# Optimization experiments

Measured on AMD Instinct MI355X. Metric: run time of the kernel, lower is better.

## Reference

```python
import jax, jax.numpy as jnp
import numpy as np

N = 729        # problem variables
B = 8          # batch
K = 32         # mixing rank (hard-coded in MixingFunc)
NB = 40        # number of symmetry-basis matrices
MAX_ITER = 10  # coordinate-descent sweeps


def setup_inputs() -> dict:
    key = jax.random.key(0)
    ks = jax.random.split(key, 7)
    coeff = jax.random.normal(ks[0], (NB,), jnp.float32)
    upper = jax.random.normal(ks[1], (N,), jnp.float32)
    basis = jax.random.normal(ks[2], (NB, N, N), jnp.float32)
    z = jax.random.uniform(ks[3], (B, N), jnp.float32)
    is_input = jax.random.randint(ks[4], (B, N), 0, 2).astype(jnp.int32)
    v_init_raw = jax.random.normal(ks[5], (B, N + 1, K), jnp.float32)
    # random permutation of the N non-truth variables (indices 1..N), as in satnet init
    perm = (jax.random.permutation(ks[6], N) + 1).astype(jnp.int32)
    return dict(coeff=coeff, upper=upper, basis=basis, z=z,
                is_input=is_input, v_init_raw=v_init_raw, perm=perm)


def _build_C(coeff, upper, basis):
    # BasisFunc.forward: C = [[0, upper^T], [upper, sum_b coeff_b * basis_b]]
    center = jnp.einsum('b,bij->ij', coeff, basis)              # (N, N)
    top = jnp.concatenate([jnp.zeros((1,), upper.dtype), upper])[None, :]  # (1, N+1)
    bottom = jnp.concatenate([upper[:, None], center], axis=1)  # (N, N+1)
    return jnp.concatenate([top, bottom], axis=0)               # (N+1, N+1)


def _init_V(v_raw, z_full):
    # SATNet init: v0 = random unit truth direction; each v_i is placed on the
    # cone around v0 at angle pi*z_i using a random orthogonal direction.
    v0 = v_raw[:, 0] / jnp.linalg.norm(v_raw[:, 0], axis=-1, keepdims=True)  # (B, K)
    dot = jnp.einsum('bnk,bk->bn', v_raw, v0)
    u = v_raw - dot[..., None] * v0[:, None, :]
    u = u / jnp.maximum(jnp.linalg.norm(u, axis=-1, keepdims=True), 1e-8)
    c = jnp.cos(jnp.pi * z_full)[..., None]
    s = jnp.sin(jnp.pi * z_full)[..., None]
    V = -c * v0[:, None, :] + s * u                              # (B, N+1, K)
    V = V.at[:, 0].set(v0)                                       # truth vector pinned
    return V


def _mix(C, V, is_input_full, perm):
    # SATNet mixing coordinate descent: for each free variable i,
    #   g_i = sum_j C[j,i] v_j - C[i,i] v_i ;  v_i <- -g_i / ||g_i||
    Cdiag = jnp.diagonal(C)
    free = (is_input_full == 0)                                  # (B, N+1)

    def coord_step(V, i):
        g = jnp.einsum('j,bjk->bk', C[:, i], V) - Cdiag[i] * V[:, i]  # (B, K)
        gn = jnp.linalg.norm(g, axis=-1, keepdims=True)
        vnew = -g / jnp.maximum(gn, 1e-8)
        V = V.at[:, i].set(jnp.where(free[:, i][:, None], vnew, V[:, i]))
        return V, None

    def sweep(V, _):
        V, _ = jax.lax.scan(coord_step, V, perm)
        return V, None

    V, _ = jax.lax.scan(jax.checkpoint(sweep), V, None, length=MAX_ITER)
    return V


def reference(coeff, upper, basis, z, is_input, v_init_raw, perm):
    Bn = z.shape[0]
    C = _build_C(coeff, upper, basis)
    z_full = jnp.concatenate([jnp.ones((Bn, 1), z.dtype), z], axis=1)
    ii_full = jnp.concatenate(
        [jnp.ones((Bn, 1), is_input.dtype), is_input], axis=1)
    V = _init_V(v_init_raw, z_full)
    V = _mix(C, V, ii_full, perm)
    v0 = V[:, 0]
    cosang = jnp.clip(-jnp.einsum('bnk,bk->bn', V, v0), -1.0 + 1e-6, 1.0 - 1e-6)
    zo = jnp.arccos(cosang) / jnp.pi
    z_out = jnp.where(ii_full == 1, z_full, zo)
    return z_out[:, 1:]
```

## Files before the change

kernel.cpp:

```cpp
#include <hip/hip_runtime.h>

#define NN   729
#define NF   730
#define BV   8
#define KK   32
#define NBAS 40
#define MAXIT 10
#define PI_F 3.14159265358979323846f

#define MTH   512
#define BT    16
#define AST   448
#define NMT   28

typedef short v8s __attribute__((ext_vector_type(8)));
typedef float v4f __attribute__((ext_vector_type(4)));

__device__ __forceinline__ unsigned short f2bf(float f) {
    unsigned int x = __float_as_uint(f);
    unsigned int r = x + 0x7FFFu + ((x >> 16) & 1u);
    return (unsigned short)(r >> 16);
}

__global__ void build_C_kernel(const float* __restrict__ coeff,
                               const float* __restrict__ upper,
                               const float* __restrict__ basis,
                               float* __restrict__ Ct) {
    int idx = blockIdx.x * blockDim.x + threadIdx.x;
    if (idx >= NF * NF) return;
    int i = idx / NF, j = idx - i * NF;
    float val;
    if (i == 0) {
        val = (j == 0) ? 0.f : upper[j - 1];
    } else if (j == 0) {
        val = upper[i - 1];
    } else {
        float acc = 0.f;
        const float* bp = basis + (size_t)(i - 1) * NN + (j - 1);
        #pragma unroll 8
        for (int b = 0; b < NBAS; ++b)
            acc = fmaf(coeff[b], bp[(size_t)b * NN * NN], acc);
        val = acc;
    }
    Ct[(size_t)j * NF + i] = val;
}

__global__ void init_V_kernel(const float* __restrict__ z,
                              const float* __restrict__ vraw,
                              float* __restrict__ V) {
    int g = threadIdx.x >> 5;
    int k = threadIdx.x & 31;
    int row = blockIdx.x * 8 + g;
    int b = row / NF, n = row - b * NF;
    const float* vr = vraw + (size_t)b * NF * KK;

    float v0 = vr[k];
    float s2 = v0 * v0;
    #pragma unroll
    for (int off = 16; off; off >>= 1) s2 += __shfl_xor(s2, off, 32);
    v0 = v0 / sqrtf(s2);

    float vn = vr[(size_t)n * KK + k];
    float d = vn * v0;
    #pragma unroll
    for (int off = 16; off; off >>= 1) d += __shfl_xor(d, off, 32);
    float u = vn - d * v0;
    float un2 = u * u;
    #pragma unroll
    for (int off = 16; off; off >>= 1) un2 += __shfl_xor(un2, off, 32);
    u = u / fmaxf(sqrtf(un2), 1e-8f);

    float zf = (n == 0) ? 1.f : z[b * NN + (n - 1)];
    float c = cosf(PI_F * zf), s = sinf(PI_F * zf);
    float outv = -c * v0 + s * u;
    if (n == 0) outv = v0;
    V[((size_t)b * NF + n) * KK + k] = outv;
}

__global__ void build_act_kernel(const int* __restrict__ is_input,
                                 const int* __restrict__ perm,
                                 int* __restrict__ act, int* __restrict__ nA_arr) {
    int b = blockIdx.x, l = threadIdx.x;
    int base = 0;
    for (int c = 0; c < (NN + 63) / 64; ++c) {
        int idx = c * 64 + l;
        bool f = false; int pi = 0;
        if (idx < NN) { pi = perm[idx]; f = (is_input[b * NN + pi - 1] == 0); }
        unsigned long long m = __ballot(f);
        int pos = __popcll(m & ((1ull << l) - 1ull));
        if (f && base + pos < AST) act[b * AST + base + pos] = pi;
        base += __popcll(m);
    }
    if (base > AST) base = AST;
    if (l == 0) nA_arr[b] = base;
    for (int p = base + l; p < AST; p += 64) act[b * AST + p] = 0;
}

__global__ void init_W_kernel(const float* __restrict__ Ct,
                              const int* __restrict__ act,
                              const int* __restrict__ nA_arr,
                              const float* __restrict__ V,
                              float* __restrict__ Wc,
                              float* __restrict__ Vact) {
    int b = blockIdx.y;
    int a = blockIdx.x * 8 + (threadIdx.x >> 5);
    int k = threadIdx.x & 31;
    int nA = nA_arr[b];
    float w = 0.f;
    int ra = act[b * AST + a];
    float vv = V[((size_t)b * NF + ra) * KK + k];
    if (a < nA) {
        const float* ctr = Ct + (size_t)ra * NF;
        const float* vb = V + (size_t)b * NF * KK + k;
        float acc = 0.f;
        for (int j = 0; j < NF; ++j)
            acc = fmaf(ctr[j], vb[(size_t)j * KK], acc);
        w = acc - ctr[ra] * vv;
    }
    Wc[((size_t)b * AST + a) * KK + k] = w;
    Vact[((size_t)b * AST + a) * KK + k] = vv;
}

__global__ void prepack_A_kernel(const float* __restrict__ Ct,
                                 const int* __restrict__ act,
                                 v8s* __restrict__ Apack) {
    int b = blockIdx.y, pm = blockIdx.x;
    int pb = pm / NMT, mt = pm - NMT * pb;
    int l = threadIdx.x;
    if (l >= 32) return;
    int row = mt * 16 + (l & 15);
    int ra = act[b * AST + row];
    const float* crow = Ct + (size_t)ra * NF;
    v8s v;
    #pragma unroll
    for (int i = 0; i < 8; ++i) {
        int t = (l >> 4) * 8 + i;
        int rt = act[b * AST + pb * 16 + t];
        v[i] = (short)f2bf(crow[rt]);
    }
    Apack[(((size_t)b * NMT + pb) * NMT + mt) * 32 + l] = v;
}

__device__ __forceinline__ float rowsum16(float x) {
    int y;
    y = __builtin_amdgcn_update_dpp(0, __float_as_int(x), 0x121, 0xF, 0xF, false);
    x += __int_as_float(y);
    y = __builtin_amdgcn_update_dpp(0, __float_as_int(x), 0x122, 0xF, 0xF, false);
    x += __int_as_float(y);
    y = __builtin_amdgcn_update_dpp(0, __float_as_int(x), 0x124, 0xF, 0xF, false);
    x += __int_as_float(y);
    y = __builtin_amdgcn_update_dpp(0, __float_as_int(x), 0x128, 0xF, 0xF, false);
    x += __int_as_float(y);
    return x;
}

__global__ __launch_bounds__(MTH, 2)
void mix_kernel(const v8s* __restrict__ Apack_g,
                const float* __restrict__ Ct_g,
                const float* __restrict__ Wc_g,
                const float* __restrict__ Vact_g,
                const int* __restrict__ act_g,
                const int* __restrict__ nA_arr,
                const int* __restrict__ is_input,
                const float* __restrict__ z,
                const float* __restrict__ Vg,
                float* __restrict__ out) {
    __shared__ __align__(16) float V_c[AST * KK];
    __shared__ __align__(16) float dv_s[2][BT * KK];
    __shared__ __align__(16) float gpub[2][BT * KK];
    __shared__ __align__(16) float cblk_s[2][BT * BT];
    __shared__ __align__(16) float cmini_s[BT * BT];
    __shared__ float Cd_s[AST];
    __shared__ int   slot_s[NF];
    __shared__ int   act_s[AST];

    int b = blockIdx.x, tid = threadIdx.x;
    const v8s* Apack = Apack_g + ((size_t)b * NMT * NMT) * 32;
    const float* Vact = Vact_g + (size_t)b * AST * KK;
    int nA = nA_arr[b];
    int nblkp = (nA + BT - 1) / BT;
    if (nblkp < 2) nblkp = 2;
    if (nblkp > NMT) nblkp = NMT;
    int totB = MAXIT * nblkp;

    int wid = tid >> 6;
    int l64 = tid & 63;
    int col = l64 & 15, rg = l64 >> 4;
    int k32 = tid & 31;

    if (tid < AST) act_s[tid] = act_g[b * AST + tid];
    __syncthreads();
    for (int idx = tid; idx < AST * 8; idx += MTH)
        ((float4*)V_c)[idx] = ((const float4*)Vact)[idx];
    if (tid < AST) Cd_s[tid] = Ct_g[(size_t)act_s[tid] * NF + act_s[tid]];
    if (tid < nA) slot_s[act_s[tid]] = tid;
    if (tid < 256) {
        int t = tid >> 4, u = tid & 15;
        cblk_s[0][t * BT + u] = Ct_g[(size_t)act_s[u] * NF + act_s[t]];
    }
    v4f acc[4][2];
    #pragma unroll
    for (int tl = 0; tl < 4; ++tl)
        #pragma unroll
        for (int nt = 0; nt < 2; ++nt) {
            v4f z4 = {0.f, 0.f, 0.f, 0.f};
            acc[tl][nt] = z4;
        }
    if (wid >= 1) {
        #pragma unroll
        for (int tl = 0; tl < 4; ++tl) {
            int mt = (wid - 1) * 4 + tl;
            #pragma unroll
            for (int nt = 0; nt < 2; ++nt)
                #pragma unroll
                for (int i = 0; i < 4; ++i)
                    acc[tl][nt][i] =
                        Wc_g[((size_t)b * AST + mt * 16 + rg * 4 + i) * KK + nt * 16 + col];
        }
        if (wid == 1) {
            #pragma unroll
            for (int nt = 0; nt < 2; ++nt)
                #pragma unroll
                for (int i = 0; i < 4; ++i)
                    gpub[1][(rg * 4 + i) * KK + nt * 16 + col] = acc[0][nt][i];
        }
    }
    __syncthreads();

    for (int bi = 0; bi < totB; ++bi) {
        int blk = bi % nblkp, s0 = blk * BT;
        int pblk = (bi - 1 + nblkp) % nblkp, sp0 = pblk * BT;
        int cb = bi & 1, pv = cb ^ 1;
        int nblk2 = (bi + 1) % nblkp, sn0 = nblk2 * BT;

        if (wid == 0) {
            __builtin_amdgcn_s_setprio(1);
            float g[BT], vo[BT];
            #pragma unroll
            for (int u = 0; u < BT; ++u) {
                g[u]  = gpub[pv][u * KK + k32];
                vo[u] = V_c[(s0 + u) * KK + k32];
            }
            #pragma unroll
            for (int u = 0; u < BT; ++u) {
                int s = s0 + u;
                float n2 = g[u] * g[u];
                n2 = rowsum16(n2);
                n2 += __shfl_xor(n2, 16, 32);
                float inv = -__builtin_amdgcn_rsqf(fmaxf(n2, 1e-16f));
                float msk = (s < nA) ? 1.f : 0.f;
                float d = fmaf(g[u], inv, -vo[u]) * msk;
                if (tid < 32) {
                    dv_s[cb][u * KK + k32] = d;
                    V_c[s * KK + k32] = vo[u] + d;
                }
                #pragma unroll
                for (int u2 = u + 1; u2 < BT; ++u2)
                    g[u2] = fmaf(cblk_s[cb][u * BT + u2], d, g[u2]);
            }
            __builtin_amdgcn_s_setprio(0);
        } else {
            if (wid == 6) {
                for (int idx = l64; idx < BT * BT; idx += 64) {
                    int u = idx >> 4, t = idx & 15;
                    cmini_s[u * BT + t] =
                        Ct_g[(size_t)act_s[sn0 + u] * NF + act_s[s0 + t]];
                }
            }
            if (wid == 7) {
                for (int idx = l64; idx < BT * BT; idx += 64) {
                    int x = idx >> 4, y = idx & 15;
                    cblk_s[pv][idx] =
                        Ct_g[(size_t)act_s[sn0 + y] * NF + act_s[sn0 + x]];
                }
            }
            if (bi > 0) {
                v8s bf0, bf1;
                #pragma unroll
                for (int i = 0; i < 8; ++i) { bf0[i] = 0; bf1[i] = 0; }
                if (l64 < 32) {
                    #pragma unroll
                    for (int i = 0; i < 8; ++i) {
                        int t = rg * 8 + i;
                        bf0[i] = (short)f2bf(dv_s[pv][t * KK + col]);
                        bf1[i] = (short)f2bf(dv_s[pv][t * KK + 16 + col]);
                    }
                }
                #pragma unroll
                for (int tl = 0; tl < 4; ++tl) {
                    int mt = (wid - 1) * 4 + tl;
                    v8s af;
                    #pragma unroll
                    for (int i = 0; i < 8; ++i) af[i] = 0;
                    if (l64 < 32)
                        af = Apack[((size_t)pblk * NMT + mt) * 32 + l64];
                    acc[tl][0] = __builtin_amdgcn_mfma_f32_16x16x32_bf16(af, bf0, acc[tl][0], 0, 0, 0);
                    acc[tl][1] = __builtin_amdgcn_mfma_f32_16x16x32_bf16(af, bf1, acc[tl][1], 0, 0, 0);
                }
                #pragma unroll
                for (int tl = 0; tl < 4; ++tl) {
                    if ((wid - 1) * 4 + tl == pblk) {
                        #pragma unroll
                        for (int i = 0; i < 4; ++i) {
                            int r = rg * 4 + i;
                            float cd = Cd_s[sp0 + r];
                            acc[tl][0][i] = fmaf(-cd, dv_s[pv][r * KK + col],      acc[tl][0][i]);
                            acc[tl][1][i] = fmaf(-cd, dv_s[pv][r * KK + 16 + col], acc[tl][1][i]);
                        }
                    }
                }
            }
            #pragma unroll
            for (int tl = 0; tl < 4; ++tl) {
                if ((wid - 1) * 4 + tl == nblk2) {
                    #pragma unroll
                    for (int i = 0; i < 4; ++i) {
                        gpub[cb][(rg * 4 + i) * KK + col]      = acc[tl][0][i];
                        gpub[cb][(rg * 4 + i) * KK + 16 + col] = acc[tl][1][i];
                    }
                }
            }
        }
        __syncthreads();

        {
            int u = tid >> 5, k = tid & 31;
            float g = gpub[cb][u * KK + k];
            #pragma unroll
            for (int t = 0; t < BT; ++t)
                g = fmaf(cmini_s[u * BT + t], dv_s[cb][t * KK + k], g);
            gpub[cb][u * KK + k] = g;
        }
        __syncthreads();
    }

    int k = tid & 31, r = tid >> 5;
    float v0k = Vg[(size_t)b * NF * KK + k];
    for (int n = 1 + r; n <= NN; n += 16) {
        int ii = is_input[b * NN + n - 1];
        float res;
        if (ii == 1) {
            res = z[b * NN + n - 1];
        } else {
            int a = slot_s[n];
            float dot = V_c[a * KK + k] * v0k;
            #pragma unroll
            for (int off = 16; off; off >>= 1) dot += __shfl_xor(dot, off, 32);
            float ca = fminf(fmaxf(-dot, -1.f + 1e-6f), 1.f - 1e-6f);
            res = acosf(ca) * (1.f / PI_F);
        }
        if (k == 0) out[b * NN + n - 1] = res;
    }
}

extern "C" void kernel_launch(void* const* d_in, const int* in_sizes, int n_in,
                              void* d_out, int out_size, void* d_ws, size_t ws_size,
                              hipStream_t stream) {
    const float* coeff    = (const float*)d_in[0];
    const float* upper    = (const float*)d_in[1];
    const float* basis    = (const float*)d_in[2];
    const float* z        = (const float*)d_in[3];
    const int*   is_input = (const int*)d_in[4];
    const float* vraw     = (const float*)d_in[5];
    const int*   perm     = (const int*)d_in[6];
    float* out = (float*)d_out;

    float* ws   = (float*)d_ws;
    float* Ct   = ws;
    float* V    = Ct + (size_t)NF * NF;
    float* Wc   = V + (size_t)BV * NF * KK;
    float* Vact = Wc + (size_t)BV * AST * KK;
    int*   act  = (int*)(Vact + (size_t)BV * AST * KK);
    int*   nAa  = act + BV * AST;
    v8s*  Apack = (v8s*)(nAa + 8);

    build_C_kernel<<<dim3((NF * NF + 255) / 256), dim3(256), 0, stream>>>(coeff, upper, basis, Ct);
    init_V_kernel<<<dim3(730), dim3(256), 0, stream>>>(z, vraw, V);
    build_act_kernel<<<dim3(BV), dim3(64), 0, stream>>>(is_input, perm, act, nAa);
    init_W_kernel<<<dim3(AST / 8, BV), dim3(256), 0, stream>>>(Ct, act, nAa, V, Wc, Vact);
    prepack_A_kernel<<<dim3(NMT * NMT, BV), dim3(64), 0, stream>>>(Ct, act, Apack);
    mix_kernel<<<dim3(BV), dim3(MTH), 0, stream>>>(Apack, Ct, Wc, Vact, act, nAa, is_input, z, V, out);
}
```

Measured before the change: 722.5 us.

## Double the coordinate-block size to 32 so MFMA uses full K width

Raises the sequential coordinate block from 16 to 32 variables, halving the number of block iterations and the __syncthreads barriers per sweep. The A-panel prepack now fills all 64 lanes, so the 16x16x32 bf16 MFMA uses its full K=32 instead of zero-padding half of it. The serial wave-0 update also now streams V values one ahead instead of holding a 16-entry array. In exchange, wave 0's serial triangular update loop per block doubles in length, the correction step handles two rows per thread, and the cblk and cmini tiles grow fourfold.

```diff
diff --git a/kernel.cpp b/kernel.cpp
--- a/kernel.cpp
+++ b/kernel.cpp
@@ -9,9 +9,10 @@
 #define PI_F 3.14159265358979323846f
 
 #define MTH   512
-#define BT    16
+#define BT    32
 #define AST   448
 #define NMT   28
+#define NPB   14
 
 typedef short v8s __attribute__((ext_vector_type(8)));
 typedef float v4f __attribute__((ext_vector_type(4)));
@@ -127,18 +128,17 @@
     int b = blockIdx.y, pm = blockIdx.x;
     int pb = pm / NMT, mt = pm - NMT * pb;
     int l = threadIdx.x;
-    if (l >= 32) return;
     int row = mt * 16 + (l & 15);
     int ra = act[b * AST + row];
     const float* crow = Ct + (size_t)ra * NF;
     v8s v;
     #pragma unroll
     for (int i = 0; i < 8; ++i) {
-        int t = (l >> 4) * 8 + i;
-        int rt = act[b * AST + pb * 16 + t];
+        int k = (l >> 4) * 8 + i;
+        int rt = act[b * AST + pb * 32 + k];
         v[i] = (short)f2bf(crow[rt]);
     }
-    Apack[(((size_t)b * NMT + pb) * NMT + mt) * 32 + l] = v;
+    Apack[(((size_t)b * NPB + pb) * NMT + mt) * 64 + l] = v;
 }
 
 __device__ __forceinline__ float rowsum16(float x) {
@@ -175,12 +175,12 @@
     __shared__ int   act_s[AST];
 
     int b = blockIdx.x, tid = threadIdx.x;
-    const v8s* Apack = Apack_g + ((size_t)b * NMT * NMT) * 32;
+    const v8s* Apack = Apack_g + ((size_t)b * NPB * NMT) * 64;
     const float* Vact = Vact_g + (size_t)b * AST * KK;
     int nA = nA_arr[b];
     int nblkp = (nA + BT - 1) / BT;
     if (nblkp < 2) nblkp = 2;
-    if (nblkp > NMT) nblkp = NMT;
+    if (nblkp > NPB) nblkp = NPB;
     int totB = MAXIT * nblkp;
 
     int wid = tid >> 6;
@@ -194,9 +194,9 @@
         ((float4*)V_c)[idx] = ((const float4*)Vact)[idx];
     if (tid < AST) Cd_s[tid] = Ct_g[(size_t)act_s[tid] * NF + act_s[tid]];
     if (tid < nA) slot_s[act_s[tid]] = tid;
-    if (tid < 256) {
-        int t = tid >> 4, u = tid & 15;
-        cblk_s[0][t * BT + u] = Ct_g[(size_t)act_s[u] * NF + act_s[t]];
+    for (int idx = tid; idx < BT * BT; idx += MTH) {
+        int x = idx >> 5, y = idx & 31;
+        cblk_s[0][idx] = Ct_g[(size_t)act_s[y] * NF + act_s[x]];
     }
     v4f acc[4][2];
     #pragma unroll
@@ -219,10 +219,12 @@
         }
         if (wid == 1) {
             #pragma unroll
-            for (int nt = 0; nt < 2; ++nt)
-                #pragma unroll
-                for (int i = 0; i < 4; ++i)
-                    gpub[1][(rg * 4 + i) * KK + nt * 16 + col] = acc[0][nt][i];
+            for (int tl = 0; tl < 2; ++tl)
+                #pragma unroll
+                for (int nt = 0; nt < 2; ++nt)
+                    #pragma unroll
+                    for (int i = 0; i < 4; ++i)
+                        gpub[1][(tl * 16 + rg * 4 + i) * KK + nt * 16 + col] = acc[tl][nt][i];
         }
     }
     __syncthreads();
@@ -235,41 +237,42 @@
 
         if (wid == 0) {
             __builtin_amdgcn_s_setprio(1);
-            float g[BT], vo[BT];
-            #pragma unroll
-            for (int u = 0; u < BT; ++u) {
-                g[u]  = gpub[pv][u * KK + k32];
-                vo[u] = V_c[(s0 + u) * KK + k32];
-            }
+            float g[BT];
+            #pragma unroll
+            for (int u = 0; u < BT; ++u)
+                g[u] = gpub[pv][u * KK + k32];
+            float vo = V_c[s0 * KK + k32];
             #pragma unroll
             for (int u = 0; u < BT; ++u) {
                 int s = s0 + u;
+                float von = (u + 1 < BT) ? V_c[(s + 1) * KK + k32] : 0.f;
                 float n2 = g[u] * g[u];
                 n2 = rowsum16(n2);
                 n2 += __shfl_xor(n2, 16, 32);
                 float inv = -__builtin_amdgcn_rsqf(fmaxf(n2, 1e-16f));
                 float msk = (s < nA) ? 1.f : 0.f;
-                float d = fmaf(g[u], inv, -vo[u]) * msk;
+                float d = fmaf(g[u], inv, -vo) * msk;
                 if (tid < 32) {
                     dv_s[cb][u * KK + k32] = d;
-                    V_c[s * KK + k32] = vo[u] + d;
+                    V_c[s * KK + k32] = vo + d;
                 }
                 #pragma unroll
                 for (int u2 = u + 1; u2 < BT; ++u2)
                     g[u2] = fmaf(cblk_s[cb][u * BT + u2], d, g[u2]);
+                vo = von;
             }
             __builtin_amdgcn_s_setprio(0);
         } else {
             if (wid == 6) {
                 for (int idx = l64; idx < BT * BT; idx += 64) {
-                    int u = idx >> 4, t = idx & 15;
-                    cmini_s[u * BT + t] =
+                    int u = idx >> 5, t = idx & 31;
+                    cmini_s[idx] =
                         Ct_g[(size_t)act_s[sn0 + u] * NF + act_s[s0 + t]];
                 }
             }
             if (wid == 7) {
                 for (int idx = l64; idx < BT * BT; idx += 64) {
-                    int x = idx >> 4, y = idx & 15;
+                    int x = idx >> 5, y = idx & 31;
                     cblk_s[pv][idx] =
                         Ct_g[(size_t)act_s[sn0 + y] * NF + act_s[sn0 + x]];
                 }
@@ -277,46 +280,41 @@
             if (bi > 0) {
                 v8s bf0, bf1;
                 #pragma unroll
-                for (int i = 0; i < 8; ++i) { bf0[i] = 0; bf1[i] = 0; }
-                if (l64 < 32) {
-                    #pragma unroll
-                    for (int i = 0; i < 8; ++i) {
-                        int t = rg * 8 + i;
-                        bf0[i] = (short)f2bf(dv_s[pv][t * KK + col]);
-                        bf1[i] = (short)f2bf(dv_s[pv][t * KK + 16 + col]);
-                    }
+                for (int i = 0; i < 8; ++i) {
+                    int t = rg * 8 + i;
+                    bf0[i] = (short)f2bf(dv_s[pv][t * KK + col]);
+                    bf1[i] = (short)f2bf(dv_s[pv][t * KK + 16 + col]);
                 }
                 #pragma unroll
                 for (int tl = 0; tl < 4; ++tl) {
                     int mt = (wid - 1) * 4 + tl;
-                    v8s af;
-                    #pragma unroll
-                    for (int i = 0; i < 8; ++i) af[i] = 0;
-                    if (l64 < 32)
-                        af = Apack[((size_t)pblk * NMT + mt) * 32 + l64];
+                    v8s af = Apack[((size_t)pblk * NMT + mt) * 64 + l64];
                     acc[tl][0] = __builtin_amdgcn_mfma_f32_16x16x32_bf16(af, bf0, acc[tl][0], 0, 0, 0);
                     acc[tl][1] = __builtin_amdgcn_mfma_f32_16x16x32_bf16(af, bf1, acc[tl][1], 0, 0, 0);
                 }
                 #pragma unroll
                 for (int tl = 0; tl < 4; ++tl) {
-                    if ((wid - 1) * 4 + tl == pblk) {
+                    int mt = (wid - 1) * 4 + tl;
+                    if ((mt >> 1) == pblk) {
                         #pragma unroll
                         for (int i = 0; i < 4; ++i) {
-                            int r = rg * 4 + i;
-                            float cd = Cd_s[sp0 + r];
-                            acc[tl][0][i] = fmaf(-cd, dv_s[pv][r * KK + col],      acc[tl][0][i]);
-                            acc[tl][1][i] = fmaf(-cd, dv_s[pv][r * KK + 16 + col], acc[tl][1][i]);
+                            int rb = (mt & 1) * 16 + rg * 4 + i;
+                            float cd = Cd_s[mt * 16 + rg * 4 + i];
+                            acc[tl][0][i] = fmaf(-cd, dv_s[pv][rb * KK + col],      acc[tl][0][i]);
+                            acc[tl][1][i] = fmaf(-cd, dv_s[pv][rb * KK + 16 + col], acc[tl][1][i]);
                         }
                     }
                 }
             }
             #pragma unroll
             for (int tl = 0; tl < 4; ++tl) {
-                if ((wid - 1) * 4 + tl == nblk2) {
+                int mt = (wid - 1) * 4 + tl;
+                if ((mt >> 1) == nblk2) {
+                    int rb0 = (mt & 1) * 16;
                     #pragma unroll
                     for (int i = 0; i < 4; ++i) {
-                        gpub[cb][(rg * 4 + i) * KK + col]      = acc[tl][0][i];
-                        gpub[cb][(rg * 4 + i) * KK + 16 + col] = acc[tl][1][i];
+                        gpub[cb][(rb0 + rg * 4 + i) * KK + col]      = acc[tl][0][i];
+                        gpub[cb][(rb0 + rg * 4 + i) * KK + 16 + col] = acc[tl][1][i];
                     }
                 }
             }
@@ -324,12 +322,17 @@
         __syncthreads();
 
         {
-            int u = tid >> 5, k = tid & 31;
-            float g = gpub[cb][u * KK + k];
-            #pragma unroll
-            for (int t = 0; t < BT; ++t)
-                g = fmaf(cmini_s[u * BT + t], dv_s[cb][t * KK + k], g);
-            gpub[cb][u * KK + k] = g;
+            int k = tid & 31;
+            int u0 = tid >> 5;
+            #pragma unroll
+            for (int uu = 0; uu < 2; ++uu) {
+                int u = u0 + 16 * uu;
+                float g = gpub[cb][u * KK + k];
+                #pragma unroll
+                for (int t = 0; t < BT; ++t)
+                    g = fmaf(cmini_s[u * BT + t], dv_s[cb][t * KK + k], g);
+                gpub[cb][u * KK + k] = g;
+            }
         }
         __syncthreads();
     }
@@ -378,6 +381,6 @@
     init_V_kernel<<<dim3(730), dim3(256), 0, stream>>>(z, vraw, V);
     build_act_kernel<<<dim3(BV), dim3(64), 0, stream>>>(is_input, perm, act, nAa);
     init_W_kernel<<<dim3(AST / 8, BV), dim3(256), 0, stream>>>(Ct, act, nAa, V, Wc, Vact);
-    prepack_A_kernel<<<dim3(NMT * NMT, BV), dim3(64), 0, stream>>>(Ct, act, Apack);
+    prepack_A_kernel<<<dim3(NPB * NMT, BV), dim3(64), 0, stream>>>(Ct, act, Apack);
     mix_kernel<<<dim3(BV), dim3(MTH), 0, stream>>>(Apack, Ct, Wc, Vact, act, nAa, is_input, z, V, out);
 }
```

Result: slower. 1.362 ms (+88.6%).

## Fold cross-block correction into serial wave, remove second barrier per block

Applied to the files above, without the earlier changes.

The separate all-thread pass that added the previous block's cmini*dv correction to the published gradients is removed, and with it one __syncthreads per block iteration. Wave 0 now applies that correction itself at the start of the next block, using a double-buffered cmini_s and the previous dv_s. V_c loads are also software-pipelined one row ahead to cut register pressure. This halves the barriers on the serial critical path but adds 256 FMAs per lane to the latency-bound wave 0.

```diff
diff --git a/kernel.cpp b/kernel.cpp
--- a/kernel.cpp
+++ b/kernel.cpp
@@ -169,7 +169,7 @@
     __shared__ __align__(16) float dv_s[2][BT * KK];
     __shared__ __align__(16) float gpub[2][BT * KK];
     __shared__ __align__(16) float cblk_s[2][BT * BT];
-    __shared__ __align__(16) float cmini_s[BT * BT];
+    __shared__ __align__(16) float cmini_s[2][BT * BT];
     __shared__ float Cd_s[AST];
     __shared__ int   slot_s[NF];
     __shared__ int   act_s[AST];
@@ -235,35 +235,47 @@
 
         if (wid == 0) {
             __builtin_amdgcn_s_setprio(1);
-            float g[BT], vo[BT];
-            #pragma unroll
-            for (int u = 0; u < BT; ++u) {
-                g[u]  = gpub[pv][u * KK + k32];
-                vo[u] = V_c[(s0 + u) * KK + k32];
-            }
+            float g[BT], dvp[BT];
+            #pragma unroll
+            for (int u = 0; u < BT; ++u)
+                g[u] = gpub[pv][u * KK + k32];
+            if (bi > 0) {
+                #pragma unroll
+                for (int t = 0; t < BT; ++t)
+                    dvp[t] = dv_s[pv][t * KK + k32];
+            } else {
+                #pragma unroll
+                for (int t = 0; t < BT; ++t) dvp[t] = 0.f;
+            }
+            float vo = V_c[s0 * KK + k32];
             #pragma unroll
             for (int u = 0; u < BT; ++u) {
                 int s = s0 + u;
+                float von = (u + 1 < BT) ? V_c[(s + 1) * KK + k32] : 0.f;
+                #pragma unroll
+                for (int t = 0; t < BT; ++t)
+                    g[u] = fmaf(cmini_s[pv][u * BT + t], dvp[t], g[u]);
                 float n2 = g[u] * g[u];
                 n2 = rowsum16(n2);
                 n2 += __shfl_xor(n2, 16, 32);
                 float inv = -__builtin_amdgcn_rsqf(fmaxf(n2, 1e-16f));
                 float msk = (s < nA) ? 1.f : 0.f;
-                float d = fmaf(g[u], inv, -vo[u]) * msk;
+                float d = fmaf(g[u], inv, -vo) * msk;
                 if (tid < 32) {
                     dv_s[cb][u * KK + k32] = d;
-                    V_c[s * KK + k32] = vo[u] + d;
+                    V_c[s * KK + k32] = vo + d;
                 }
                 #pragma unroll
                 for (int u2 = u + 1; u2 < BT; ++u2)
                     g[u2] = fmaf(cblk_s[cb][u * BT + u2], d, g[u2]);
+                vo = von;
             }
             __builtin_amdgcn_s_setprio(0);
         } else {
             if (wid == 6) {
                 for (int idx = l64; idx < BT * BT; idx += 64) {
                     int u = idx >> 4, t = idx & 15;
-                    cmini_s[u * BT + t] =
+                    cmini_s[cb][u * BT + t] =
                         Ct_g[(size_t)act_s[sn0 + u] * NF + act_s[s0 + t]];
                 }
             }
@@ -320,16 +332,6 @@
                     }
                 }
             }
-        }
-        __syncthreads();
-
-        {
-            int u = tid >> 5, k = tid & 31;
-            float g = gpub[cb][u * KK + k];
-            #pragma unroll
-            for (int t = 0; t < BT; ++t)
-                g = fmaf(cmini_s[u * BT + t], dv_s[cb][t * KK + k], g);
-            gpub[cb][u * KK + k] = g;
         }
         __syncthreads();
     }
```

Result: slower. 896.2 us (+24.0%).
